# Optimization experiments

Measured on AMD Instinct MI355X. Metric: run time of the kernel, lower is better.

## Reference

```python
import jax, jax.numpy as jnp
import numpy as np

B, D_IN, D_OUT = 8192, 4096, 4096
IN_DIMS = (64, 64)
OUT_DIMS = (64, 64)
# tt_rank_rate=0.5 over dims [64,64,64,64] -> ranks [1,32,1024,32,1]
RANKS = (1, 32, 1024, 32, 1)


def _kaiming_uniform(key, shape):
    # matches nn.init.kaiming_uniform_(a=sqrt(5)) on a (r_prev, d, r) tensor:
    # fan_in = prod(shape[1:]) = d * r, gain = sqrt(2/(1+5)) = sqrt(1/3)
    fan_in = shape[1] * shape[2]
    bound = np.sqrt(1.0 / 3.0) * np.sqrt(3.0 / fan_in)
    return jax.random.uniform(key, shape, jnp.float32, -bound, bound)


def setup_inputs() -> dict:
    key = jax.random.key(0)
    kx, k0, k1, k2, k3, kb = jax.random.split(key, 6)
    dims = list(IN_DIMS) + list(OUT_DIMS)
    shapes = [(RANKS[i], dims[i], RANKS[i + 1]) for i in range(4)]
    x = jax.random.normal(kx, (B, D_IN), jnp.float32)
    core0 = _kaiming_uniform(k0, shapes[0])  # (1, 64, 32)
    core1 = _kaiming_uniform(k1, shapes[1])  # (32, 64, 1024)
    core2 = _kaiming_uniform(k2, shapes[2])  # (1024, 64, 32)
    core3 = _kaiming_uniform(k3, shapes[3])  # (32, 64, 1)
    bb = 1.0 / np.sqrt(D_IN)
    bias = jax.random.uniform(kb, (D_OUT,), jnp.float32, -bb, bb)
    return {"x": x, "core0": core0, "core1": core1, "core2": core2,
            "core3": core3, "bias": bias}


def reference(x, core0, core1, core2, core3, bias):
    b = x.shape[0]
    s = x.reshape(b, IN_DIMS[0], IN_DIMS[1])          # (B, 64, 64)
    # input core 0: contract first input dim (rank-in = 1 squeezed)
    s = jnp.einsum('bcd,cs->bds', s, core0[0])        # (B, 64, 32)
    # input core 1: contract second input dim and rank
    s = jnp.einsum('bcr,rcs->bs', s, core1)           # (B, 1024)
    # output core 2: expand first output dim
    s = jnp.einsum('br,rAs->bAs', s, core2)           # (B, 64, 32)
    # output core 3: expand second output dim (rank-out = 1 squeezed)
    s = jnp.einsum('bAr,rB->bAB', s, core3[..., 0])   # (B, 64, 64)
    return s.reshape(b, -1) + bias                    # (B, 4096)
```

## Files before the change

### kernel.cpp

```cpp
#include <hip/hip_runtime.h>
#include <hip/hip_bf16.h>


typedef _Float16 h4 __attribute__((ext_vector_type(4)));
typedef _Float16 h8 __attribute__((ext_vector_type(8)));
typedef float f32x4 __attribute__((ext_vector_type(4)));

#define BATCH 8192

__device__ __forceinline__ void gld_lds16(const void* g, void* l) {
  __builtin_amdgcn_global_load_lds(
      (__attribute__((address_space(1))) void*)(g),
      (__attribute__((address_space(3))) void*)(l), 16, 0, 0);
}

__global__ __launch_bounds__(256) void transpose_cast2(
    const float* __restrict__ c1, _Float16* __restrict__ W1t,
    const float* __restrict__ c2, _Float16* __restrict__ W2t) {
  __shared__ float t[64][65];
  const int which = blockIdx.z;
  const float* src = which ? c2 : c1;
  _Float16* dst = which ? W2t : W1t;
  const int K = which ? 1024 : 2048, U = which ? 2048 : 1024;
  const int k0 = (which ? blockIdx.y : blockIdx.x) * 64;
  const int u0 = (which ? blockIdx.x : blockIdx.y) * 64;
  const int tx = threadIdx.x & 63, ty = threadIdx.x >> 6;
  for (int i = ty; i < 64; i += 4) {
    const int k = k0 + i;
    const int sr = which ? k : ((k & 31) * 64 + (k >> 5));
    t[i][tx] = src[(size_t)sr * U + u0 + tx];
  }
  __syncthreads();
  for (int i = ty; i < 64; i += 4) {
    dst[(size_t)(u0 + i) * K + k0 + tx] = (_Float16)t[tx][i];
  }
}

__global__ __launch_bounds__(256) void stage2(const float* __restrict__ x,
                                              const float* __restrict__ c0,
                                              _Float16* __restrict__ s1) {
  __shared__ _Float16 xh[4 * 4096];
  __shared__ float c0l[2048];
  const int b0 = blockIdx.x * 4;
  const int tid = threadIdx.x;

  {
    const float4* xg = (const float4*)(x + (size_t)b0 * 4096);
#pragma unroll
    for (int k = 0; k < 16; ++k) {
      float4 v = xg[tid + 256 * k];
      h4 w = {(_Float16)v.x, (_Float16)v.y, (_Float16)v.z, (_Float16)v.w};
      ((h4*)xh)[tid + 256 * k] = w;
    }
    ((float4*)c0l)[tid] = ((const float4*)c0)[tid];
    ((float4*)c0l)[tid + 256] = ((const float4*)c0)[tid + 256];
  }
  __syncthreads();

  const int row = tid >> 6, t6 = tid & 63;
  const int d0 = (t6 >> 3) * 8;
  const int r0 = (t6 & 7) * 4;
  const _Float16* xrow = xh + row * 4096;

  float acc[8][4];
#pragma unroll
  for (int i = 0; i < 8; ++i)
#pragma unroll
    for (int j = 0; j < 4; ++j) acc[i][j] = 0.0f;

  for (int c = 0; c < 64; ++c) {
    h8 xv = *(const h8*)&xrow[c * 64 + d0];
    f32x4 wv = *(const f32x4*)&c0l[c * 32 + r0];
#pragma unroll
    for (int i = 0; i < 8; ++i) {
      const float xf = (float)xv[i];
#pragma unroll
      for (int j = 0; j < 4; ++j) acc[i][j] += xf * wv[j];
    }
  }

  _Float16* s1row = s1 + (size_t)(b0 + row) * 2048;
#pragma unroll
  for (int i = 0; i < 8; ++i) {
    h4 o = {(_Float16)acc[i][0], (_Float16)acc[i][1], (_Float16)acc[i][2],
            (_Float16)acc[i][3]};
    *(h4*)&s1row[(d0 + i) * 32 + r0] = o;
  }
}

template <int K, int CN, bool FUSED>
__global__ __launch_bounds__(512, 2) void gemm_pipe(
    const _Float16* __restrict__ A, const _Float16* __restrict__ Bt,
    _Float16* __restrict__ C, const float* __restrict__ c3,
    const float* __restrict__ bias, float* __restrict__ out) {
  __shared__ __align__(16) char lds[3 * 49152];
  constexpr int NT = K / 64;
  const int bm = blockIdx.x, bn = blockIdx.y;
  const int tid = threadIdx.x;
  const int w = tid >> 6, lane = tid & 63;
  const int lr = lane & 15, kh = lane >> 4;
  const int wmo = (w >> 2) << 6, wno = (w & 3) << 6;

  f32x4 acc[4][4] = {};

  const int sr = tid >> 3;
  const int sc = ((tid & 7) ^ (sr & 7)) << 4;
  const char* gA = (const char*)(A + (size_t)(bm * 128 + sr) * K) + sc;
  const char* gB = (const char*)(Bt + (size_t)(bn * 256 + sr) * K) + sc;
  const size_t rk = (size_t)K * 128;
  char* lw = lds + (w << 10);

  auto STAGE_A = [&](int t) {
    char* b_ = lw + (t % 3) * 49152;
    const char* ga = gA + (size_t)t * 128;
    gld_lds16(ga, b_);
    gld_lds16(ga + rk, b_ + 8192);
    gld_lds16(gB + (size_t)t * 128, b_ + 16384);
  };
  auto STAGE_B = [&](int t) {
    char* b_ = lw + (t % 3) * 49152;
    const char* gb = gB + (size_t)t * 128;
    gld_lds16(gb + rk, b_ + 24576);
    gld_lds16(gb + 2 * rk, b_ + 32768);
    gld_lds16(gb + 3 * rk, b_ + 40960);
  };

  auto KTILE = [&](int t, bool last) {
    if (last)
      asm volatile("s_waitcnt vmcnt(0)" ::: "memory");
    else
      asm volatile("s_waitcnt vmcnt(6)" ::: "memory");
    __builtin_amdgcn_s_barrier();
    __builtin_amdgcn_sched_barrier(0);
    const char* bufA = lds + (t % 3) * 49152;
    const char* bufB = bufA + 16384;
    h8 af[2][4], bf[2][4];
#pragma unroll
    for (int kk = 0; kk < 2; ++kk) {
#pragma unroll
      for (int m = 0; m < 4; ++m) {
        const int R = wmo + m * 16 + lr;
        af[kk][m] = *(const h8*)(bufA + R * 128 +
                                 ((((kk << 2) + kh) ^ (R & 7)) << 4));
      }
#pragma unroll
      for (int n = 0; n < 2; ++n) {
        const int R = wno + n * 16 + lr;
        bf[kk][n] = *(const h8*)(bufB + R * 128 +
                                 ((((kk << 2) + kh) ^ (R & 7)) << 4));
      }
    }
    if (t + 2 < NT) STAGE_A(t + 2);
    asm volatile("s_waitcnt lgkmcnt(0)" ::: "memory");
    __builtin_amdgcn_sched_barrier(0);
    __builtin_amdgcn_s_setprio(1);
#pragma unroll
    for (int kk = 0; kk < 2; ++kk)
#pragma unroll
      for (int m = 0; m < 4; ++m)
#pragma unroll
        for (int n = 0; n < 2; ++n)
          acc[m][n] = __builtin_amdgcn_mfma_f32_16x16x32_f16(
              af[kk][m], bf[kk][n], acc[m][n], 0, 0, 0);
    __builtin_amdgcn_s_setprio(0);
    __builtin_amdgcn_s_barrier();
    __builtin_amdgcn_sched_barrier(0);
#pragma unroll
    for (int kk = 0; kk < 2; ++kk)
#pragma unroll
      for (int n = 2; n < 4; ++n) {
        const int R = wno + n * 16 + lr;
        bf[kk][n] = *(const h8*)(bufB + R * 128 +
                                 ((((kk << 2) + kh) ^ (R & 7)) << 4));
      }
    if (t + 2 < NT) STAGE_B(t + 2);
    asm volatile("s_waitcnt lgkmcnt(0)" ::: "memory");
    __builtin_amdgcn_sched_barrier(0);
    __builtin_amdgcn_s_setprio(1);
#pragma unroll
    for (int kk = 0; kk < 2; ++kk)
#pragma unroll
      for (int m = 0; m < 4; ++m)
#pragma unroll
        for (int n = 2; n < 4; ++n)
          acc[m][n] = __builtin_amdgcn_mfma_f32_16x16x32_f16(
              af[kk][m], bf[kk][n], acc[m][n], 0, 0, 0);
    __builtin_amdgcn_s_setprio(0);
  };

  STAGE_A(0); STAGE_B(0);
  STAGE_A(1); STAGE_B(1);
  for (int t = 0; t < NT - 1; ++t) KTILE(t, false);
  KTILE(NT - 1, true);

  if constexpr (!FUSED) {
#pragma unroll
    for (int m = 0; m < 4; ++m) {
      const int r0 = bm * 128 + wmo + m * 16 + kh * 4;
#pragma unroll
      for (int n = 0; n < 4; ++n) {
        const int c0 = bn * 256 + wno + n * 16 + lr;
#pragma unroll
        for (int q = 0; q < 4; ++q)
          C[(size_t)(r0 + q) * CN + c0] = (_Float16)acc[m][n][q];
      }
    }
  } else {
    h8 bfe[4];
    float bb[8][4];
#pragma unroll
    for (int n = 0; n < 4; ++n) {
#pragma unroll
      for (int j = 0; j < 8; ++j)
        bfe[n][j] = (_Float16)c3[(kh * 8 + j) * 64 + n * 16 + lr];
#pragma unroll
      for (int a = 0; a < 8; ++a)
        bb[a][n] = bias[(bn * 8 + a) * 64 + n * 16 + lr];
    }
    __syncthreads();
#pragma unroll
    for (int m = 0; m < 4; ++m) {
      const int Rb = wmo + m * 16 + kh * 4;
#pragma unroll
      for (int n = 0; n < 4; ++n) {
        const int cc = wno + n * 16 + lr;
#pragma unroll
        for (int q = 0; q < 4; ++q) {
          const int R = Rb + q;
          *(_Float16*)(lds + R * 512 +
                       ((((cc >> 3) ^ (R & 7)) << 4) | ((cc & 7) << 1))) =
              (_Float16)acc[m][n][q];
        }
      }
    }
    __syncthreads();
    const int row = (w << 4) + lr;
    const int orow0 = bm * 128 + (w << 4) + (kh << 2);
#pragma unroll
    for (int a = 0; a < 8; ++a) {
      h8 afv = *(const h8*)(lds + row * 512 +
                            ((((a << 2) + kh) ^ (row & 7)) << 4));
#pragma unroll
      for (int n = 0; n < 4; ++n) {
        f32x4 d = {};
        d = __builtin_amdgcn_mfma_f32_16x16x32_f16(afv, bfe[n], d, 0, 0, 0);
        const int ocol = (bn * 8 + a) * 64 + n * 16 + lr;
#pragma unroll
        for (int q = 0; q < 4; ++q)
          out[(size_t)(orow0 + q) * 4096 + ocol] = d[q] + bb[a][n];
      }
    }
  }
}

extern "C" void kernel_launch(void* const* d_in, const int* in_sizes, int n_in,
                              void* d_out, int out_size, void* d_ws,
                              size_t ws_size, hipStream_t stream) {
  (void)in_sizes; (void)n_in; (void)out_size; (void)ws_size;
  const float* x     = (const float*)d_in[0];
  const float* core0 = (const float*)d_in[1];
  const float* core1 = (const float*)d_in[2];
  const float* core2 = (const float*)d_in[3];
  const float* core3 = (const float*)d_in[4];
  const float* bias  = (const float*)d_in[5];
  float* out = (float*)d_out;

  char* ws = (char*)d_ws;
  _Float16* s1h = (_Float16*)ws;
  _Float16* s2h = (_Float16*)(ws + 33554432);
  _Float16* W1t = (_Float16*)(ws + 50331648);
  _Float16* W2t = (_Float16*)(ws + 54525952);

  transpose_cast2<<<dim3(32, 16, 2), 256, 0, stream>>>(core1, W1t, core2, W2t);
  stage2<<<BATCH / 4, 256, 0, stream>>>(x, core0, s1h);
  gemm_pipe<2048, 1024, false><<<dim3(BATCH / 128, 4), 512, 0, stream>>>(
      s1h, W1t, s2h, nullptr, nullptr, nullptr);
  gemm_pipe<1024, 4096, true><<<dim3(BATCH / 128, 8), 512, 0, stream>>>(
      s2h, W2t, nullptr, core3, bias, out);
}
```

Baseline: 151.6 us.

## Use 256x256 tiles with BK=32 triple-buffered pipeline for second GEMM

New measurement: 153.5 us. No clear change (+1.3%).

```diff
diff --git a/kernel.cpp b/kernel.cpp
--- a/kernel.cpp
+++ b/kernel.cpp
@@ -88,11 +88,10 @@
   }
 }
 
-template <int K, int CN, bool FUSED>
+template <int K, int CN>
 __global__ __launch_bounds__(512, 2) void gemm_pipe(
     const _Float16* __restrict__ A, const _Float16* __restrict__ Bt,
-    _Float16* __restrict__ C, const float* __restrict__ c3,
-    const float* __restrict__ bias, float* __restrict__ out) {
+    _Float16* __restrict__ C) {
   __shared__ __align__(16) char lds[3 * 49152];
   constexpr int NT = K / 64;
   const int bm = blockIdx.x, bn = blockIdx.y;
@@ -193,53 +192,146 @@
   for (int t = 0; t < NT - 1; ++t) KTILE(t, false);
   KTILE(NT - 1, true);
 
-  if constexpr (!FUSED) {
+#pragma unroll
+  for (int m = 0; m < 4; ++m) {
+    const int r0 = bm * 128 + wmo + m * 16 + kh * 4;
+#pragma unroll
+    for (int n = 0; n < 4; ++n) {
+      const int c0 = bn * 256 + wno + n * 16 + lr;
+#pragma unroll
+      for (int q = 0; q < 4; ++q)
+        C[(size_t)(r0 + q) * CN + c0] = (_Float16)acc[m][n][q];
+    }
+  }
+}
+
+template <int K>
+__global__ __launch_bounds__(512, 2) void gemm2_8p(
+    const _Float16* __restrict__ A, const _Float16* __restrict__ Bt,
+    const float* __restrict__ c3, const float* __restrict__ bias,
+    float* __restrict__ out) {
+  __shared__ __align__(16) char lds[131072];
+  constexpr int NT = K / 32;
+  const int bm = blockIdx.x, bn = blockIdx.y;
+  const int tid = threadIdx.x;
+  const int w = tid >> 6, lane = tid & 63;
+  const int lr = lane & 15, kh = lane >> 4;
+  const int wmo = (w >> 2) << 7;
+  const int wno = (w & 3) << 6;
+
+  f32x4 acc[8][4] = {};
+
+  const int sr = tid >> 2;
+  const int sc = ((tid & 3) ^ (sr & 3)) << 4;
+  const char* gA = (const char*)A + (size_t)(bm * 256 + sr) * (K * 2) + sc;
+  const char* gB = (const char*)Bt + (size_t)(bn * 256 + sr) * (K * 2) + sc;
+  const size_t rk128 = (size_t)128 * K * 2;
+  char* lw = lds + (w << 10);
+
+  auto STAGE_A2 = [&](int t) {
+    char* b_ = lw + (t % 3) * 32768;
+    const char* ga = gA + (size_t)t * 64;
+    gld_lds16(ga, b_);
+    gld_lds16(ga + rk128, b_ + 8192);
+  };
+  auto STAGE_B2 = [&](int t) {
+    char* b_ = lw + (t % 3) * 32768 + 16384;
+    const char* gb = gB + (size_t)t * 64;
+    gld_lds16(gb, b_);
+    gld_lds16(gb + rk128, b_ + 8192);
+  };
+
+  auto KTILE = [&](int t, bool last) {
+    if (last)
+      asm volatile("s_waitcnt vmcnt(0)" ::: "memory");
+    else
+      asm volatile("s_waitcnt vmcnt(4)" ::: "memory");
+    __builtin_amdgcn_s_barrier();
+    __builtin_amdgcn_sched_barrier(0);
+    const char* bufA = lds + (t % 3) * 32768;
+    const char* bufB = bufA + 16384;
+    h8 af[8], bf[4];
 #pragma unroll
     for (int m = 0; m < 4; ++m) {
-      const int r0 = bm * 128 + wmo + m * 16 + kh * 4;
-#pragma unroll
-      for (int n = 0; n < 4; ++n) {
-        const int c0 = bn * 256 + wno + n * 16 + lr;
-#pragma unroll
-        for (int q = 0; q < 4; ++q)
-          C[(size_t)(r0 + q) * CN + c0] = (_Float16)acc[m][n][q];
-      }
-    }
-  } else {
-    h8 bfe[4];
-    float bb[8][4];
+      const int R = wmo + m * 16 + lr;
+      af[m] = *(const h8*)(bufA + R * 64 + ((kh ^ (R & 3)) << 4));
+    }
 #pragma unroll
     for (int n = 0; n < 4; ++n) {
-#pragma unroll
-      for (int j = 0; j < 8; ++j)
-        bfe[n][j] = (_Float16)c3[(kh * 8 + j) * 64 + n * 16 + lr];
-#pragma unroll
-      for (int a = 0; a < 8; ++a)
-        bb[a][n] = bias[(bn * 8 + a) * 64 + n * 16 + lr];
-    }
-    __syncthreads();
-#pragma unroll
-    for (int m = 0; m < 4; ++m) {
-      const int Rb = wmo + m * 16 + kh * 4;
-#pragma unroll
-      for (int n = 0; n < 4; ++n) {
-        const int cc = wno + n * 16 + lr;
-#pragma unroll
-        for (int q = 0; q < 4; ++q) {
-          const int R = Rb + q;
-          *(_Float16*)(lds + R * 512 +
-                       ((((cc >> 3) ^ (R & 7)) << 4) | ((cc & 7) << 1))) =
-              (_Float16)acc[m][n][q];
-        }
-      }
-    }
-    __syncthreads();
-    const int row = (w << 4) + lr;
-    const int orow0 = bm * 128 + (w << 4) + (kh << 2);
+      const int R = wno + n * 16 + lr;
+      bf[n] = *(const h8*)(bufB + R * 64 + ((kh ^ (R & 3)) << 4));
+    }
+    if (t + 2 < NT) STAGE_A2(t + 2);
+    asm volatile("s_waitcnt lgkmcnt(0)" ::: "memory");
+    __builtin_amdgcn_sched_barrier(0);
+    __builtin_amdgcn_s_setprio(1);
+#pragma unroll
+    for (int m = 0; m < 4; ++m)
+#pragma unroll
+      for (int n = 0; n < 4; ++n)
+        acc[m][n] = __builtin_amdgcn_mfma_f32_16x16x32_f16(af[m], bf[n],
+                                                           acc[m][n], 0, 0, 0);
+    __builtin_amdgcn_s_setprio(0);
+#pragma unroll
+    for (int m = 4; m < 8; ++m) {
+      const int R = wmo + m * 16 + lr;
+      af[m] = *(const h8*)(bufA + R * 64 + ((kh ^ (R & 3)) << 4));
+    }
+    if (t + 2 < NT) STAGE_B2(t + 2);
+    asm volatile("s_waitcnt lgkmcnt(0)" ::: "memory");
+    __builtin_amdgcn_sched_barrier(0);
+    __builtin_amdgcn_s_setprio(1);
+#pragma unroll
+    for (int m = 4; m < 8; ++m)
+#pragma unroll
+      for (int n = 0; n < 4; ++n)
+        acc[m][n] = __builtin_amdgcn_mfma_f32_16x16x32_f16(af[m], bf[n],
+                                                           acc[m][n], 0, 0, 0);
+    __builtin_amdgcn_s_setprio(0);
+  };
+
+  STAGE_A2(0); STAGE_B2(0);
+  STAGE_A2(1); STAGE_B2(1);
+  for (int t = 0; t < NT - 1; ++t) KTILE(t, false);
+  KTILE(NT - 1, true);
+
+  h8 bfe[4];
+  float bb[8][4];
+#pragma unroll
+  for (int n = 0; n < 4; ++n) {
+#pragma unroll
+    for (int j = 0; j < 8; ++j)
+      bfe[n][j] = (_Float16)c3[(kh * 8 + j) * 64 + n * 16 + lr];
+#pragma unroll
+    for (int a = 0; a < 8; ++a)
+      bb[a][n] = bias[(bn * 8 + a) * 64 + n * 16 + lr];
+  }
+  __syncthreads();
+#pragma unroll
+  for (int m = 0; m < 8; ++m) {
+    const int Rb = wmo + m * 16 + kh * 4;
+#pragma unroll
+    for (int n = 0; n < 4; ++n) {
+      const int cc = wno + n * 16 + lr;
+#pragma unroll
+      for (int q = 0; q < 4; ++q) {
+        const int R = Rb + q;
+        *(_Float16*)(lds + R * 512 +
+                     ((((cc >> 3) ^ (R & 7)) << 4) | ((cc & 7) << 1))) =
+            (_Float16)acc[m][n][q];
+      }
+    }
+  }
+  __syncthreads();
+  const int r32 = w << 5;
+#pragma unroll
+  for (int mi = 0; mi < 2; ++mi) {
+    const int rr = r32 + mi * 16 + lr;
+    const int orow0 = bm * 256 + r32 + mi * 16 + (kh << 2);
 #pragma unroll
     for (int a = 0; a < 8; ++a) {
-      h8 afv = *(const h8*)(lds + row * 512 +
-                            ((((a << 2) + kh) ^ (row & 7)) << 4));
+      h8 afv = *(const h8*)(lds + rr * 512 +
+                            ((((a * 4 + kh) ^ (rr & 7)) << 4)));
 #pragma unroll
       for (int n = 0; n < 4; ++n) {
         f32x4 d = {};
@@ -273,8 +365,6 @@
 
   transpose_cast2<<<dim3(32, 16, 2), 256, 0, stream>>>(core1, W1t, core2, W2t);
   stage2<<<BATCH / 4, 256, 0, stream>>>(x, core0, s1h);
-  gemm_pipe<2048, 1024, false><<<dim3(BATCH / 128, 4), 512, 0, stream>>>(
-      s1h, W1t, s2h, nullptr, nullptr, nullptr);
-  gemm_pipe<1024, 4096, true><<<dim3(BATCH / 128, 8), 512, 0, stream>>>(
-      s2h, W2t, nullptr, core3, bias, out);
-}
+  gemm_pipe<2048, 1024><<<dim3(BATCH / 128, 4), 512, 0, stream>>>(s1h, W1t, s2h);
+  gemm2_8p<1024><<<dim3(BATCH / 256, 8), 512, 0, stream>>>(s2h, W2t, core3, bias, out);
+}
```

## Load stage2 inputs directly to LDS as fp32 and halve rows per block

Applied to the files above, without the earlier changes.

After: 154.8 us. 2.1% more time.

```diff
diff --git a/kernel.cpp b/kernel.cpp
--- a/kernel.cpp
+++ b/kernel.cpp
@@ -2,8 +2,10 @@
 #include <hip/hip_bf16.h>
 
 
+typedef _Float16 h2 __attribute__((ext_vector_type(2)));
 typedef _Float16 h4 __attribute__((ext_vector_type(4)));
 typedef _Float16 h8 __attribute__((ext_vector_type(8)));
+typedef float f32x2 __attribute__((ext_vector_type(2)));
 typedef float f32x4 __attribute__((ext_vector_type(4)));
 
 #define BATCH 8192
@@ -39,52 +41,45 @@
 __global__ __launch_bounds__(256) void stage2(const float* __restrict__ x,
                                               const float* __restrict__ c0,
                                               _Float16* __restrict__ s1) {
-  __shared__ _Float16 xh[4 * 4096];
-  __shared__ float c0l[2048];
-  const int b0 = blockIdx.x * 4;
+  __shared__ __align__(16) float xf[2 * 4096];
+  __shared__ __align__(16) float c0l[2048];
+  const int b0 = blockIdx.x * 2;
   const int tid = threadIdx.x;
+  const int w = tid >> 6;
 
   {
-    const float4* xg = (const float4*)(x + (size_t)b0 * 4096);
-#pragma unroll
-    for (int k = 0; k < 16; ++k) {
-      float4 v = xg[tid + 256 * k];
-      h4 w = {(_Float16)v.x, (_Float16)v.y, (_Float16)v.z, (_Float16)v.w};
-      ((h4*)xh)[tid + 256 * k] = w;
-    }
-    ((float4*)c0l)[tid] = ((const float4*)c0)[tid];
-    ((float4*)c0l)[tid + 256] = ((const float4*)c0)[tid + 256];
+    const char* gx = (const char*)(x + (size_t)b0 * 4096) + (size_t)tid * 16;
+    char* lx = (char*)xf + (w << 10);
+#pragma unroll
+    for (int r = 0; r < 8; ++r) gld_lds16(gx + r * 4096, lx + r * 4096);
+    const char* gc = (const char*)c0 + (size_t)tid * 16;
+    char* lc = (char*)c0l + (w << 10);
+#pragma unroll
+    for (int r = 0; r < 2; ++r) gld_lds16(gc + r * 4096, lc + r * 4096);
   }
   __syncthreads();
 
-  const int row = tid >> 6, t6 = tid & 63;
-  const int d0 = (t6 >> 3) * 8;
-  const int r0 = (t6 & 7) * 4;
-  const _Float16* xrow = xh + row * 4096;
-
-  float acc[8][4];
-#pragma unroll
-  for (int i = 0; i < 8; ++i)
-#pragma unroll
-    for (int j = 0; j < 4; ++j) acc[i][j] = 0.0f;
-
+  const int row = tid >> 7, t7 = tid & 127;
+  const int d0 = (t7 >> 4) * 8;
+  const int r0 = (t7 & 15) * 2;
+  const float* xrow = xf + row * 4096;
+
+  f32x4 acc[2][2] = {};
   for (int c = 0; c < 64; ++c) {
-    h8 xv = *(const h8*)&xrow[c * 64 + d0];
-    f32x4 wv = *(const f32x4*)&c0l[c * 32 + r0];
-#pragma unroll
-    for (int i = 0; i < 8; ++i) {
-      const float xf = (float)xv[i];
-#pragma unroll
-      for (int j = 0; j < 4; ++j) acc[i][j] += xf * wv[j];
-    }
+    f32x4 x0 = *(const f32x4*)&xrow[c * 64 + d0];
+    f32x4 x1 = *(const f32x4*)&xrow[c * 64 + d0 + 4];
+    f32x2 wv = *(const f32x2*)&c0l[c * 32 + r0];
+    acc[0][0] += x0 * wv[0];
+    acc[0][1] += x1 * wv[0];
+    acc[1][0] += x0 * wv[1];
+    acc[1][1] += x1 * wv[1];
   }
 
   _Float16* s1row = s1 + (size_t)(b0 + row) * 2048;
 #pragma unroll
   for (int i = 0; i < 8; ++i) {
-    h4 o = {(_Float16)acc[i][0], (_Float16)acc[i][1], (_Float16)acc[i][2],
-            (_Float16)acc[i][3]};
-    *(h4*)&s1row[(d0 + i) * 32 + r0] = o;
+    h2 o = {(_Float16)acc[0][i >> 2][i & 3], (_Float16)acc[1][i >> 2][i & 3]};
+    *(h2*)&s1row[(d0 + i) * 32 + r0] = o;
   }
 }
 
@@ -272,7 +267,7 @@
   _Float16* W2t = (_Float16*)(ws + 54525952);
 
   transpose_cast2<<<dim3(32, 16, 2), 256, 0, stream>>>(core1, W1t, core2, W2t);
-  stage2<<<BATCH / 4, 256, 0, stream>>>(x, core0, s1h);
+  stage2<<<BATCH / 2, 256, 0, stream>>>(x, core0, s1h);
   gemm_pipe<2048, 1024, false><<<dim3(BATCH / 128, 4), 512, 0, stream>>>(
       s1h, W1t, s2h, nullptr, nullptr, nullptr);
   gemm_pipe<1024, 4096, true><<<dim3(BATCH / 128, 8), 512, 0, stream>>>(
```
